# Performance work log

Hardware: AMD Instinct MI355X
Metric: run time of the kernel (lower is better)

The kernel has to match this reference:

```python
import jax, jax.numpy as jnp
import numpy as np

N = 65536      # total nodes (cells) in batch
E = 262144     # edges per edge type
T = 3          # edge types: row, col, diag
D = 128        # hidden_dim
HG = 4         # gat_heads
DHG = D // HG  # 32, GAT head dim
HH = 4         # hgt_heads
DHH = D // HH  # 32, HGT head dim
B = 32         # boards per batch
SLOPE = 0.2
EPS = 1e-6


def setup_inputs():
    ks = jax.random.split(jax.random.key(0), 32)
    def nrm(i, shape, s=0.05):
        return (jax.random.normal(ks[i], shape) * s).astype(jnp.float32)
    inp = {
        'x_cell': nrm(0, (N, D), 1.0),
        'z_h': nrm(1, (B, D), 1.0),
        'x_cell_embedded': nrm(2, (N, D), 1.0),
        'edge_index': jax.random.randint(ks[3], (T, 2, E), 0, N, dtype=jnp.int32),
        'batch_size': B,
        # GAT conv 1 (one GATConv per edge type, summed)
        'gat1_W': nrm(4, (T, D, D), 0.09),
        'gat1_asrc': nrm(5, (T, HG, DHG), 0.12),
        'gat1_adst': nrm(6, (T, HG, DHG), 0.12),
        'gat1_b': jnp.zeros((T, D), jnp.float32),
        # GAT conv 2
        'gat2_W': nrm(7, (T, D, D), 0.09),
        'gat2_asrc': nrm(8, (T, HG, DHG), 0.12),
        'gat2_adst': nrm(9, (T, HG, DHG), 0.12),
        'gat2_b': jnp.zeros((T, D), jnp.float32),
        # RMSNorms
        'norm1_s': jnp.ones((D,), jnp.float32),
        'norm2_s': jnp.ones((D,), jnp.float32),
        'norm3_s': jnp.ones((D,), jnp.float32),
        # HGT (single node type 'cell', T edge types)
        'hgt_Wk': nrm(10, (D, D), 0.09), 'hgt_bk': jnp.zeros((D,), jnp.float32),
        'hgt_Wq': nrm(11, (D, D), 0.09), 'hgt_bq': jnp.zeros((D,), jnp.float32),
        'hgt_Wv': nrm(12, (D, D), 0.09), 'hgt_bv': jnp.zeros((D,), jnp.float32),
        'hgt_arel': nrm(13, (T, HH, DHH, DHH), 0.15),
        'hgt_mrel': nrm(14, (T, HH, DHH, DHH), 0.15),
        'hgt_prel': jnp.ones((T, HH), jnp.float32),
        'hgt_Wo': nrm(15, (D, D), 0.09), 'hgt_bo': jnp.zeros((D,), jnp.float32),
        'hgt_skip': jnp.ones((), jnp.float32),
        # input injection
        'inj_W': nrm(16, (D, D), 0.09), 'inj_b': jnp.zeros((D,), jnp.float32),
        # FiLM
        'film_W1': nrm(17, (D, 2 * D), 0.09), 'film_b1': jnp.zeros((2 * D,), jnp.float32),
        'film_W2': nrm(18, (2 * D, 2 * D), 0.001), 'film_b2': jnp.zeros((2 * D,), jnp.float32),
    }
    return inp


def _rmsnorm(x, scale):
    return scale * x * jax.lax.rsqrt(jnp.mean(x * x, axis=-1, keepdims=True) + EPS)


def _res(x_old, x_new, scale):
    return jax.nn.leaky_relu(x_old + _rmsnorm(x_new, scale), SLOPE)


def _gat_sum(x, W, asrc, adst, b, src, dst):
    """HeteroConv(sum) over T GATConvs (concat heads, add_self_loops)."""
    loop = jnp.arange(N, dtype=src.dtype)
    def one(Wt, a_s, a_d, bt, s, t):
        s = jnp.concatenate([s, loop])   # self loops
        t = jnp.concatenate([t, loop])
        h = (x @ Wt).reshape(N, HG, DHG)             # [N,H,Dh]
        alpha_src = (h * a_s).sum(-1)                # [N,H]
        alpha_dst = (h * a_d).sum(-1)
        e = jax.nn.leaky_relu(alpha_src[s] + alpha_dst[t], SLOPE)  # [E+N,H]
        m = jax.ops.segment_max(e, t, num_segments=N)
        ex = jnp.exp(e - m[t])
        denom = jax.ops.segment_sum(ex, t, num_segments=N)
        alpha = ex / (denom[t] + 1e-16)
        out = jax.ops.segment_sum(alpha[:, :, None] * h[s], t, num_segments=N)
        return out.reshape(N, D) + bt
    return jax.vmap(one)(W, asrc, adst, b, src, dst).sum(0)


def _hgt(x, Wk, bk, Wq, bq, Wv, bv, a_rel, m_rel, p_rel, Wo, bo, skip, src, dst):
    k = (x @ Wk + bk).reshape(N, HH, DHH)
    q = (x @ Wq + bq).reshape(N, HH, DHH)
    v = (x @ Wv + bv).reshape(N, HH, DHH)
    # per-edge-type relation transforms at node level, then gather per edge
    k_t = jnp.einsum('nhd,thdf->tnhf', k, a_rel)    # [T,N,H,Dk]
    v_t = jnp.einsum('nhd,thdf->tnhf', v, m_rel)
    k_e = jax.vmap(lambda a, i: a[i])(k_t, src)     # [T,E,H,Dk]
    v_e = jax.vmap(lambda a, i: a[i])(v_t, src)
    score = (q[dst] * k_e).sum(-1) * p_rel[:, None, :] / np.sqrt(DHH)  # [T,E,H]
    score = score.reshape(T * E, HH)
    dst_f = dst.reshape(-1)
    m = jax.ops.segment_max(score, dst_f, num_segments=N)
    ex = jnp.exp(score - m[dst_f])
    denom = jax.ops.segment_sum(ex, dst_f, num_segments=N)
    alpha = ex / (denom[dst_f] + 1e-16)
    agg = jax.ops.segment_sum(alpha[:, :, None] * v_e.reshape(T * E, HH, DHH),
                              dst_f, num_segments=N)          # [N,H,Dk]
    out = jax.nn.gelu(agg.reshape(N, D), approximate=False) @ Wo + bo
    sig = jax.nn.sigmoid(skip)
    return sig * out + (1.0 - sig) * x


def _film(nodes, z_h, W1, b1, W2, b2, bsz):
    gb = jax.nn.gelu(z_h @ W1 + b1, approximate=False) @ W2 + b2  # [B,2D]
    gamma, beta = jnp.split(gb, 2, axis=-1)
    gamma = 0.1 * jnp.tanh(gamma)
    beta = 0.1 * jnp.tanh(beta)
    c = N // bsz
    out = (1.0 + gamma)[:, None, :] * nodes.reshape(bsz, c, D) + beta[:, None, :]
    return out.reshape(N, D)


def reference(x_cell, z_h, x_cell_embedded,
              gat1_W, gat1_asrc, gat1_adst, gat1_b,
              gat2_W, gat2_asrc, gat2_adst, gat2_b,
              norm1_s, norm2_s, norm3_s,
              hgt_Wk, hgt_bk, hgt_Wq, hgt_bq, hgt_Wv, hgt_bv,
              hgt_arel, hgt_mrel, hgt_prel, hgt_Wo, hgt_bo, hgt_skip,
              inj_W, inj_b, film_W1, film_b1, film_W2, film_b2,
              edge_index, batch_size):
    src = edge_index[:, 0]
    dst = edge_index[:, 1]
    x1 = _res(x_cell, _gat_sum(x_cell, gat1_W, gat1_asrc, gat1_adst, gat1_b, src, dst), norm1_s)
    x2 = _res(x1, _gat_sum(x1, gat2_W, gat2_asrc, gat2_adst, gat2_b, src, dst), norm2_s)
    x3 = _res(x2, _hgt(x2, hgt_Wk, hgt_bk, hgt_Wq, hgt_bq, hgt_Wv, hgt_bv,
                       hgt_arel, hgt_mrel, hgt_prel, hgt_Wo, hgt_bo, hgt_skip,
                       src, dst), norm3_s)
    x3 = x3 + x_cell_embedded @ inj_W + inj_b
    return _film(x3, z_h, film_W1, film_b1, film_W2, film_b2, batch_size)
```

## Files before the change

kernel.cpp:

```cpp
#include <hip/hip_runtime.h>

#define NN 65536
#define EE 262144
#define ND ((size_t)NN * 128)
#define TBW 132
#define WLP 136
#define NTOT (EE + NN)
#define CSRN (3*EE + 3*NN)

typedef unsigned short u16;
typedef short bf8_t __attribute__((ext_vector_type(8)));
typedef float f32x4 __attribute__((ext_vector_type(4)));

__device__ __forceinline__ float lrelu(float x){ return x > 0.f ? x : 0.2f*x; }
__device__ __forceinline__ float gelu_exact(float x){ return 0.5f*x*(1.f+erff(x*0.70710678118654752f)); }
__device__ __forceinline__ float fexp(float x){ return __expf(x); }
__device__ __forceinline__ u16 f2bf(float f){
    union { float f; unsigned u; } v; v.f = f;
    unsigned u = v.u;
    return (u16)((u + 0x7FFFu + ((u >> 16) & 1u)) >> 16);
}
__device__ __forceinline__ float bf2f(u16 b){
    union { unsigned u; float f; } v; v.u = ((unsigned)b) << 16; return v.f;
}
__device__ __forceinline__ float2 bf2x(unsigned p){
    union { unsigned u; float f; } a, b;
    a.u = (p & 0xFFFFu) << 16; b.u = p & 0xFFFF0000u;
    return make_float2(a.f, b.f);
}
__device__ __forceinline__ unsigned cvt2(float a, float b){
    unsigned r; asm("v_cvt_pk_bf16_f32 %0, %1, %2" : "=v"(r) : "v"(a), "v"(b)); return r;
}

__device__ __forceinline__ void load_af32(const float* __restrict__ X, int row, int lk, bf8_t* af){
    #pragma unroll
    for (int kk = 0; kk < 4; ++kk){
        const float* p = X + (size_t)row*128 + kk*32 + lk*8;
        float4 a = *(const float4*)p;
        float4 b = *(const float4*)(p+4);
        union { bf8_t v; unsigned u[4]; } r;
        r.u[0] = cvt2(a.x, a.y); r.u[1] = cvt2(a.z, a.w);
        r.u[2] = cvt2(b.x, b.y); r.u[3] = cvt2(b.z, b.w);
        af[kk] = r.v;
    }
}
__device__ __forceinline__ void load_af16(const u16* __restrict__ X, int row, int lk, bf8_t* af){
    #pragma unroll
    for (int kk = 0; kk < 4; ++kk)
        af[kk] = *(const bf8_t*)(X + (size_t)row*128 + kk*32 + lk*8);
}

__device__ __forceinline__ void stage_w(const u16* __restrict__ src, u16* __restrict__ wl, int tid){
    #pragma unroll
    for (int j = 0; j < 8; ++j){
        int o = (j*256 + tid)*8;
        bf8_t v = *(const bf8_t*)(src + o);
        *(bf8_t*)(wl + ((o>>7)*WLP + (o&127))) = v;
    }
}

__device__ __forceinline__ void mfma_l1_acc(const bf8_t* af, const u16* __restrict__ wl,
                                            int lr, int lk, f32x4* acc){
    #pragma unroll
    for (int kk = 0; kk < 4; ++kk){
        bf8_t B[8];
        #pragma unroll
        for (int nt = 0; nt < 8; ++nt)
            B[nt] = *(const bf8_t*)&wl[(nt*16+lr)*WLP + kk*32 + lk*8];
        #pragma unroll
        for (int nt = 0; nt < 8; ++nt)
            acc[nt] = __builtin_amdgcn_mfma_f32_16x16x32_bf16(af[kk], B[nt], acc[nt], 0, 0, 0);
    }
}
__device__ __forceinline__ void mfma_l1(const bf8_t* af, const u16* __restrict__ wl,
                                        int lr, int lk, f32x4* acc){
    #pragma unroll
    for (int i = 0; i < 8; ++i) acc[i] = (f32x4){0.f,0.f,0.f,0.f};
    mfma_l1_acc(af, wl, lr, lk, acc);
}
__device__ __forceinline__ void mfma_l2(const bf8_t* af0, const bf8_t* af1,
                                        const u16* __restrict__ wl,
                                        int lr, int lk, f32x4* acc0, f32x4* acc1){
    #pragma unroll
    for (int i = 0; i < 8; ++i){ acc0[i] = (f32x4){0.f,0.f,0.f,0.f}; acc1[i] = (f32x4){0.f,0.f,0.f,0.f}; }
    #pragma unroll
    for (int kk = 0; kk < 4; ++kk){
        bf8_t B[8];
        #pragma unroll
        for (int nt = 0; nt < 8; ++nt)
            B[nt] = *(const bf8_t*)&wl[(nt*16+lr)*WLP + kk*32 + lk*8];
        #pragma unroll
        for (int nt = 0; nt < 8; ++nt){
            acc0[nt] = __builtin_amdgcn_mfma_f32_16x16x32_bf16(af0[kk], B[nt], acc0[nt], 0, 0, 0);
            acc1[nt] = __builtin_amdgcn_mfma_f32_16x16x32_bf16(af1[kk], B[nt], acc1[nt], 0, 0, 0);
        }
    }
}

__device__ __forceinline__ void acc_to_tb(u16 (*tbw)[TBW], const f32x4* acc, int lr, int lk, const float* bias){
    asm volatile("s_waitcnt lgkmcnt(0)" ::: "memory");
    #pragma unroll
    for (int nt = 0; nt < 8; ++nt){
        int col = nt*16 + lr;
        float badd = bias ? bias[col] : 0.f;
        #pragma unroll
        for (int i = 0; i < 4; ++i) tbw[lk*4+i][col] = f2bf(acc[nt][i] + badd);
    }
    asm volatile("s_waitcnt lgkmcnt(0)" ::: "memory");
}
__device__ __forceinline__ void acc_to_tb_gelu(u16 (*tbw)[TBW], const f32x4* acc, int lr, int lk){
    asm volatile("s_waitcnt lgkmcnt(0)" ::: "memory");
    #pragma unroll
    for (int nt = 0; nt < 8; ++nt){
        int col = nt*16 + lr;
        #pragma unroll
        for (int i = 0; i < 4; ++i) tbw[lk*4+i][col] = f2bf(gelu_exact(acc[nt][i]));
    }
    asm volatile("s_waitcnt lgkmcnt(0)" ::: "memory");
}
__device__ __forceinline__ void tb_store(const u16 (*tbw)[TBW], u16* __restrict__ O, size_t rowstride, int rowbase, int lr, int lk){
    #pragma unroll
    for (int c = 0; c < 4; ++c){
        bf8_t v = *(const bf8_t*)&tbw[c*4+lk][lr*8];
        *(bf8_t*)(O + (size_t)(rowbase + c*4 + lk)*rowstride + lr*8) = v;
    }
}
__device__ __forceinline__ void tb_frags(const u16 (*tbw)[TBW], int lr, int lk, bf8_t* ha){
    #pragma unroll
    for (int kk = 0; kk < 4; ++kk) ha[kk] = *(const bf8_t*)&tbw[lr][kk*32 + lk*8];
}
__device__ __forceinline__ void tb_rows(const u16 (*tbw)[TBW], int lr, int lk, bf8_t* rw){
    #pragma unroll
    for (int c = 0; c < 4; ++c) rw[c] = *(const bf8_t*)&tbw[c*4+lk][lr*8];
}

__global__ __launch_bounds__(256) void wpack_k(
    const float* __restrict__ g1W, const float* __restrict__ g2W,
    const float* __restrict__ Wk, const float* __restrict__ Wq, const float* __restrict__ Wv,
    const float* __restrict__ Wo, const float* __restrict__ injW,
    const float* __restrict__ arel, const float* __restrict__ mrel,
    const float* __restrict__ g1as, const float* __restrict__ g1ad,
    const float* __restrict__ g2as, const float* __restrict__ g2ad,
    u16* __restrict__ wp, u16* __restrict__ wpa)
{
    int b = blockIdx.x, tid = threadIdx.x;
    if (b < 17) {
        const float* src; int rel = 0;
        if (b < 3) src = g1W + b*16384;
        else if (b < 6) src = g2W + (b-3)*16384;
        else if (b == 6) src = Wk;
        else if (b == 7) src = Wq;
        else if (b == 8) src = Wv;
        else if (b == 9) src = Wo;
        else if (b == 10) src = injW;
        else if (b < 14) { src = arel + (b-11)*4096; rel = 2; }
        else { src = mrel + (b-14)*4096; rel = 1; }
        u16* dst = wp + (size_t)b*16384;
        for (int idx = tid; idx < 16384; idx += 256) {
            int n = idx >> 7, k = idx & 127;
            float v;
            if (rel == 1)      v = ((n>>5)==(k>>5)) ? src[(n>>5)*1024 + (k&31)*32 + (n&31)] : 0.f;
            else if (rel == 2) v = ((n>>5)==(k>>5)) ? src[(n>>5)*1024 + (n&31)*32 + (k&31)] : 0.f;
            else               v = src[k*128 + n];
            dst[idx] = f2bf(v);
        }
    } else {
        for (int idx = tid; idx < 6*2048; idx += 256) {
            int m = idx >> 11;
            int j = idx & 2047;
            int cg = j >> 7, k = j & 127;
            const float* as = (m < 3) ? g1as : g2as;
            const float* ad = (m < 3) ? g1ad : g2ad;
            int t = (m < 3) ? m : m - 3;
            float v = 0.f;
            if (cg < 4)      { if ((k>>5)==cg)   v = as[t*128 + cg*32 + (k&31)]; }
            else if (cg < 8) { int g = cg-4; if ((k>>5)==g) v = ad[t*128 + g*32 + (k&31)]; }
            wpa[idx] = f2bf(v);
        }
    }
}

template<int AF32>
__global__ __launch_bounds__(256, 3) void gat_gemm3_k(const float* __restrict__ Xf, const u16* __restrict__ Xb,
    const u16* __restrict__ wpg, const u16* __restrict__ wpa,
    u16* __restrict__ hb, float* __restrict__ alsb, float* __restrict__ aldb)
{
    __shared__ __align__(16) u16 wl[128*WLP];
    __shared__ __align__(16) u16 tb[4][16][TBW];
    const int tid = threadIdx.x, wave = tid>>6, lane = tid&63, lr = lane&15, lk = lane>>4;
    const int t = blockIdx.y;
    const int rw0 = blockIdx.x*128 + wave*32;
    bf8_t af0[4], af1[4];
    if (AF32){ load_af32(Xf, rw0 + lr, lk, af0); load_af32(Xf, rw0 + 16 + lr, lk, af1); }
    else     { load_af16(Xb, rw0 + lr, lk, af0); load_af16(Xb, rw0 + 16 + lr, lk, af1); }
    stage_w(wpg + t*16384, wl, tid);
    bf8_t Ba[4];
    #pragma unroll
    for (int kk = 0; kk < 4; ++kk)
        Ba[kk] = *(const bf8_t*)&wpa[t*2048 + lr*128 + kk*32 + lk*8];
    __syncthreads();
    f32x4 acc0[8], acc1[8];
    mfma_l2(af0, af1, wl, lr, lk, acc0, acc1);
    u16* h = hb + (size_t)t*ND;
    float* alst = alsb + (size_t)t*NN*4;
    float* aldt = aldb + (size_t)t*NN*4;
    {
        acc_to_tb(tb[wave], acc0, lr, lk, nullptr);
        tb_store(tb[wave], h, 128, rw0, lr, lk);
        bf8_t ha[4]; tb_frags(tb[wave], lr, lk, ha);
        f32x4 a2 = (f32x4){0.f,0.f,0.f,0.f};
        #pragma unroll
        for (int kk = 0; kk < 4; ++kk)
            a2 = __builtin_amdgcn_mfma_f32_16x16x32_bf16(ha[kk], Ba[kk], a2, 0, 0, 0);
        if (lr < 8){
            float* dp = (lr < 4) ? alst : aldt;
            int g = lr & 3;
            #pragma unroll
            for (int i = 0; i < 4; ++i) dp[(size_t)(rw0 + lk*4 + i)*4 + g] = a2[i];
        }
    }
    {
        acc_to_tb(tb[wave], acc1, lr, lk, nullptr);
        tb_store(tb[wave], h, 128, rw0 + 16, lr, lk);
        bf8_t ha[4]; tb_frags(tb[wave], lr, lk, ha);
        f32x4 a2 = (f32x4){0.f,0.f,0.f,0.f};
        #pragma unroll
        for (int kk = 0; kk < 4; ++kk)
            a2 = __builtin_amdgcn_mfma_f32_16x16x32_bf16(ha[kk], Ba[kk], a2, 0, 0, 0);
        if (lr < 8){
            float* dp = (lr < 4) ? alst : aldt;
            int g = lr & 3;
            #pragma unroll
            for (int i = 0; i < 4; ++i) dp[(size_t)(rw0 + 16 + lk*4 + i)*4 + g] = a2[i];
        }
    }
}

__global__ __launch_bounds__(256, 3) void hgt_proj_k(const u16* __restrict__ X,
    const u16* __restrict__ wpk, const u16* __restrict__ wpq, const u16* __restrict__ wpv,
    const u16* __restrict__ wparel,
    const float* __restrict__ bk, const float* __restrict__ bq, const float* __restrict__ bv,
    u16* __restrict__ kvb, u16* __restrict__ qtb)
{
    __shared__ __align__(16) u16 wl[128*WLP];
    __shared__ __align__(16) u16 tb[4][16][TBW];
    const int tid = threadIdx.x, wave = tid>>6, lane = tid&63, lr = lane&15, lk = lane>>4;
    const int task = blockIdx.y;
    const int rw0 = blockIdx.x*128 + wave*32;
    bf8_t af0[4], af1[4];
    load_af16(X, rw0 + lr, lk, af0);
    load_af16(X, rw0 + 16 + lr, lk, af1);
    f32x4 acc0[8], acc1[8];
    if (task == 0) {
        stage_w(wpk, wl, tid);
        __syncthreads();
        mfma_l2(af0, af1, wl, lr, lk, acc0, acc1);
        acc_to_tb(tb[wave], acc0, lr, lk, bk); tb_store(tb[wave], kvb, 256, rw0, lr, lk);
        acc_to_tb(tb[wave], acc1, lr, lk, bk); tb_store(tb[wave], kvb, 256, rw0 + 16, lr, lk);
    } else if (task == 1) {
        stage_w(wpv, wl, tid);
        __syncthreads();
        mfma_l2(af0, af1, wl, lr, lk, acc0, acc1);
        acc_to_tb(tb[wave], acc0, lr, lk, bv); tb_store(tb[wave], kvb + 128, 256, rw0, lr, lk);
        acc_to_tb(tb[wave], acc1, lr, lk, bv); tb_store(tb[wave], kvb + 128, 256, rw0 + 16, lr, lk);
    } else {
        const int t = task - 2;
        stage_w(wpq, wl, tid);
        __syncthreads();
        mfma_l2(af0, af1, wl, lr, lk, acc0, acc1);
        bf8_t ha0[4], ha1[4];
        acc_to_tb(tb[wave], acc0, lr, lk, bq); tb_frags(tb[wave], lr, lk, ha0);
        acc_to_tb(tb[wave], acc1, lr, lk, bq); tb_frags(tb[wave], lr, lk, ha1);
        __syncthreads();
        stage_w(wparel + t*16384, wl, tid);
        __syncthreads();
        mfma_l2(ha0, ha1, wl, lr, lk, acc0, acc1);
        u16* o = qtb + (size_t)t*ND;
        acc_to_tb(tb[wave], acc0, lr, lk, nullptr); tb_store(tb[wave], o, 128, rw0, lr, lk);
        acc_to_tb(tb[wave], acc1, lr, lk, nullptr); tb_store(tb[wave], o, 128, rw0 + 16, lr, lk);
    }
}

__global__ __launch_bounds__(256) void hist_k(const int* __restrict__ ei, int* __restrict__ cnt){
    int gid = blockIdx.x*256 + threadIdx.x;
    int t = gid / EE, e = gid - t*EE;
    int d = ei[t*2*EE + EE + e];
    atomicAdd(&cnt[t*NN + d], 1);
}
__global__ __launch_bounds__(256) void scanA_k(const int* __restrict__ cnt, int* __restrict__ s0off, int* __restrict__ parts){
    __shared__ int sums[256];
    int b = blockIdx.x; int base = b * 1024;
    int tid = threadIdx.x;
    int v[4]; int tsum = 0;
    #pragma unroll
    for (int i = 0; i < 4; ++i){
        int n = base + tid*4 + i;
        v[i] = cnt[n] + cnt[NN+n] + cnt[2*NN+n] + 3;
        tsum += v[i];
    }
    sums[tid] = tsum; __syncthreads();
    for (int ofs = 1; ofs < 256; ofs <<= 1) {
        int a = (tid >= ofs) ? sums[tid-ofs] : 0;
        __syncthreads();
        sums[tid] += a;
        __syncthreads();
    }
    int run = sums[tid] - tsum;
    #pragma unroll
    for (int i = 0; i < 4; ++i){ s0off[base + tid*4 + i] = run; run += v[i]; }
    if (tid == 255) parts[b] = sums[255];
}
__global__ void scan2_k(int* parts){
    if (threadIdx.x == 0 && blockIdx.x == 0) {
        int run = 0;
        for (int i = 0; i < 64; ++i) { int v = parts[i]; parts[i] = run; run += v; }
    }
}
__global__ __launch_bounds__(256) void scanB_k(const int* __restrict__ cnt, int* __restrict__ s0off,
                                               int* __restrict__ s1off, int* __restrict__ s2off,
                                               const int* __restrict__ parts){
    int b = blockIdx.x; int base = b * 1024;
    int add = parts[b];
    #pragma unroll
    for (int i = 0; i < 4; ++i){
        int n = base + threadIdx.x*4 + i;
        int m = s0off[n] + add;
        int c0 = cnt[n], c1 = cnt[NN+n];
        s0off[n] = m;
        s1off[n] = m + c0 + 1;
        s2off[n] = m + c0 + c1 + 2;
    }
    if (b == 0 && threadIdx.x == 0) s0off[NN] = CSRN;
}
__global__ __launch_bounds__(256) void selffill_k(const int* __restrict__ s0off, const int* __restrict__ s1off,
                                                  const int* __restrict__ s2off, int* __restrict__ csrc){
    int gid = blockIdx.x*256 + threadIdx.x;
    int t = gid / NN, n = gid - t*NN;
    int pos = (t==0) ? s0off[n] : (t==1 ? s1off[n] : s2off[n]);
    csrc[pos] = n;
}
__global__ __launch_bounds__(256) void scatter_k(const int* __restrict__ ei,
    const int* __restrict__ s0off, const int* __restrict__ s1off, const int* __restrict__ s2off,
    int* __restrict__ cur, int* __restrict__ csrc, int* __restrict__ posmap){
    int gid = blockIdx.x*256 + threadIdx.x;
    int t = gid / EE, e = gid - t*EE;
    int s = ei[t*2*EE + e];
    int d = ei[t*2*EE + EE + e];
    int p = atomicAdd(&cur[t*NN + d], 1);
    int basep = (t==0) ? s0off[d] : (t==1 ? s1off[d] : s2off[d]);
    int pos = basep + 1 + p;
    csrc[pos] = s;
    posmap[t*EE + e] = pos;
}

__global__ __launch_bounds__(256) void alpha_k(const float* __restrict__ alsb, const float* __restrict__ aldb,
    const int* __restrict__ ei, const int* __restrict__ posmap,
    const int* __restrict__ s0off, const int* __restrict__ s1off, const int* __restrict__ s2off,
    float4* __restrict__ ab)
{
    int gid = blockIdx.x*256 + threadIdx.x;
    int t = gid / NTOT, r = gid - t*NTOT;
    int s, d, pos;
    if (r < EE) {
        s = ei[t*2*EE + r];
        d = ei[t*2*EE + EE + r];
        pos = posmap[t*EE + r];
    } else {
        int n = r - EE;
        s = n; d = n;
        pos = (t==0) ? s0off[n] : (t==1 ? s1off[n] : s2off[n]);
    }
    const float* As = alsb + ((size_t)t*NN + s)*4;
    const float* Ad = aldb + ((size_t)t*NN + d)*4;
    float4 o;
    o.x = fexp(lrelu(As[0] + Ad[0]));
    o.y = fexp(lrelu(As[1] + Ad[1]));
    o.z = fexp(lrelu(As[2] + Ad[2]));
    o.w = fexp(lrelu(As[3] + Ad[3]));
    ab[pos] = o;
}

template<int XF32>
__global__ __launch_bounds__(256) void gat_aggres_k(const u16* __restrict__ hb,
    const float* __restrict__ abf,
    const int* __restrict__ s0off, const int* __restrict__ s1off, const int* __restrict__ s2off,
    const int* __restrict__ csrc,
    const float* __restrict__ bias3, const float* __restrict__ xoldf, const u16* __restrict__ xoldb,
    const float* __restrict__ scale, u16* __restrict__ outb)
{
    int gid = blockIdx.x*256 + threadIdx.x;
    int node = gid >> 6, lane = gid & 63;
    int g = lane >> 4;
    int segb[4] = { s0off[node], s1off[node], s2off[node], s0off[node+1] };
    float a0 = 0.f, a1 = 0.f;
    for (int t = 0; t < 3; ++t) {
        const u16* h = hb + (size_t)t*ND;
        int beg = segb[t], end = segb[t+1];
        float s0 = 0.f, s1 = 0.f, ds = 0.f;
        for (int pos = beg; pos < end; pos += 4) {
            int pc[4]; float al[4]; int sp[4]; unsigned hw[4];
            #pragma unroll
            for (int j = 0; j < 4; ++j){
                int pj = pos + j;
                pc[j] = (pj < end) ? pj : beg;
            }
            #pragma unroll
            for (int j = 0; j < 4; ++j) sp[j] = csrc[pc[j]];
            #pragma unroll
            for (int j = 0; j < 4; ++j){
                float a = abf[(size_t)pc[j]*4 + g];
                al[j] = (pos + j < end) ? a : 0.f;
                hw[j] = *(const unsigned*)&h[(size_t)sp[j]*128 + lane*2];
            }
            #pragma unroll
            for (int j = 0; j < 4; ++j){
                float2 w = bf2x(hw[j]);
                ds += al[j]; s0 += al[j]*w.x; s1 += al[j]*w.y;
            }
        }
        float inv = 1.f/(ds + 1e-16f);
        a0 += s0*inv; a1 += s1*inv;
    }
    int c0 = lane*2;
    a0 += bias3[c0]   + bias3[128+c0]   + bias3[256+c0];
    a1 += bias3[c0+1] + bias3[128+c0+1] + bias3[256+c0+1];
    float ssum = a0*a0 + a1*a1;
    #pragma unroll
    for (int o = 1; o < 64; o <<= 1) ssum += __shfl_xor(ssum, o);
    float r = rsqrtf(ssum*(1.f/128.f) + 1e-6f);
    size_t off = (size_t)node*128 + c0;
    float2 xo;
    if (XF32) xo = *(const float2*)&xoldf[off];
    else      xo = bf2x(*(const unsigned*)&xoldb[off]);
    float y0 = lrelu(xo.x + scale[c0]*a0*r);
    float y1 = lrelu(xo.y + scale[c0+1]*a1*r);
    *(unsigned*)&outb[off] = cvt2(y0, y1);
}

__global__ __launch_bounds__(256) void hgt_agg_k(const u16* __restrict__ kvb,
    const u16* __restrict__ qtb, const float* __restrict__ prel,
    const int* __restrict__ s0off, const int* __restrict__ s1off, const int* __restrict__ s2off,
    const int* __restrict__ csrc, u16* __restrict__ pb)
{
    int gid = blockIdx.x*256 + threadIdx.x;
    int node = gid >> 6, lane = gid & 63;
    int hh = lane >> 4;
    const float S = 0.17677669529663689f;
    int segb[4] = { s0off[node], s1off[node], s2off[node], s0off[node+1] };
    float dsum = 0.f;
    float a0[3], a1[3];
    for (int t = 0; t < 3; ++t) {
        a0[t] = 0.f; a1[t] = 0.f;
        float ph = prel[t*4 + hh] * S;
        float2 qv = bf2x(*(const unsigned*)&qtb[(size_t)t*ND + (size_t)node*128 + lane*2]);
        int beg = segb[t] + 1, end = segb[t+1];
        for (int pos = beg; pos < end; pos += 4) {
            int pc[4]; int sp[4]; unsigned kw[4], vw[4];
            #pragma unroll
            for (int j = 0; j < 4; ++j){
                int pj = pos + j;
                pc[j] = (pj < end) ? pj : beg;
            }
            #pragma unroll
            for (int j = 0; j < 4; ++j) sp[j] = csrc[pc[j]];
            #pragma unroll
            for (int j = 0; j < 4; ++j){
                size_t ro = (size_t)sp[j]*256 + lane*2;
                kw[j] = *(const unsigned*)&kvb[ro];
                vw[j] = *(const unsigned*)&kvb[ro + 128];
            }
            float sc[4];
            #pragma unroll
            for (int j = 0; j < 4; ++j){
                float2 k2 = bf2x(kw[j]);
                sc[j] = qv.x*k2.x + qv.y*k2.y;
            }
            #pragma unroll
            for (int o = 1; o < 16; o <<= 1){
                #pragma unroll
                for (int j = 0; j < 4; ++j) sc[j] += __shfl_xor(sc[j], o);
            }
            #pragma unroll
            for (int j = 0; j < 4; ++j){
                float ex = (pos + j < end) ? fexp(sc[j]*ph) : 0.f;
                float2 v2 = bf2x(vw[j]);
                dsum += ex; a0[t] += ex*v2.x; a1[t] += ex*v2.y;
            }
        }
    }
    float inv = 1.f/(dsum + 1e-16f);
    size_t o = (size_t)node*128 + lane*2;
    *(unsigned*)&pb[o]        = cvt2(a0[0]*inv, a1[0]*inv);
    *(unsigned*)&pb[ND + o]   = cvt2(a0[1]*inv, a1[1]*inv);
    *(unsigned*)&pb[2*ND + o] = cvt2(a0[2]*inv, a1[2]*inv);
}

__global__ __launch_bounds__(256, 3) void final_k(const u16* __restrict__ pb,
    const u16* __restrict__ wpmrel, const u16* __restrict__ wpo, const float* __restrict__ bo,
    const u16* __restrict__ x2b, const float* __restrict__ skipp, const float* __restrict__ scale,
    const float* __restrict__ xemb, const u16* __restrict__ wpinj, const float* __restrict__ injb,
    const float* __restrict__ gbuf, const int* __restrict__ bszp,
    float* __restrict__ out)
{
    __shared__ __align__(16) u16 wl[128*WLP];
    __shared__ __align__(16) u16 tb[4][16][TBW];
    const int tid = threadIdx.x, wave = tid>>6, lane = tid&63, lr = lane&15, lk = lane>>4;
    const int rw = blockIdx.x*64 + wave*16;
    f32x4 acc[8];
    #pragma unroll
    for (int i = 0; i < 8; ++i) acc[i] = (f32x4){0.f,0.f,0.f,0.f};
    for (int t = 0; t < 3; ++t){
        if (t) __syncthreads();
        bf8_t a0[4]; load_af16(pb + (size_t)t*ND, rw + lr, lk, a0);
        stage_w(wpmrel + t*16384, wl, tid);
        __syncthreads();
        mfma_l1_acc(a0, wl, lr, lk, acc);
    }
    bf8_t ga[4];
    acc_to_tb_gelu(tb[wave], acc, lr, lk);
    tb_frags(tb[wave], lr, lk, ga);
    __syncthreads();
    stage_w(wpo, wl, tid);
    __syncthreads();
    mfma_l1(ga, wl, lr, lk, acc);
    bf8_t hw[4];
    acc_to_tb(tb[wave], acc, lr, lk, bo);
    tb_rows(tb[wave], lr, lk, hw);
    bf8_t e0[4];
    load_af32(xemb, rw + lr, lk, e0);
    __syncthreads();
    stage_w(wpinj, wl, tid);
    __syncthreads();
    mfma_l1(e0, wl, lr, lk, acc);
    bf8_t in[4];
    acc_to_tb(tb[wave], acc, lr, lk, injb);
    tb_rows(tb[wave], lr, lk, in);
    const float sig = 1.f/(1.f + expf(-skipp[0]));
    const int cpb = NN / *bszp;
    float4 sca = *(const float4*)&scale[lr*8];
    float4 scb = *(const float4*)&scale[lr*8 + 4];
    #pragma unroll
    for (int c = 0; c < 4; ++c){
        int row = rw + c*4 + lk;
        bf8_t x8 = *(const bf8_t*)(x2b + (size_t)row*128 + lr*8);
        float x[8], v[8];
        float ssl = 0.f;
        #pragma unroll
        for (int j = 0; j < 8; ++j){
            x[j] = bf2f((u16)x8[j]);
            float h = bf2f((u16)hw[c][j]);
            v[j] = sig*h + (1.f - sig)*x[j];
            ssl += v[j]*v[j];
        }
        ssl += __shfl_xor(ssl, 1); ssl += __shfl_xor(ssl, 2);
        ssl += __shfl_xor(ssl, 4); ssl += __shfl_xor(ssl, 8);
        float rq = rsqrtf(ssl*(1.f/128.f) + 1e-6f);
        const float* gr = gbuf + (row / cpb)*256;
        float4 g0 = *(const float4*)&gr[lr*8];
        float4 g1 = *(const float4*)&gr[lr*8 + 4];
        float4 b0 = *(const float4*)&gr[128 + lr*8];
        float4 b1 = *(const float4*)&gr[128 + lr*8 + 4];
        float4 oA, oB;
        #pragma unroll
        for (int j = 0; j < 8; ++j){
            float scj = (j < 4) ? ((const float*)&sca)[j] : ((const float*)&scb)[j-4];
            float y = lrelu(x[j] + scj*v[j]*rq);
            float hf = y + bf2f((u16)in[c][j]);
            float gj = (j < 4) ? ((const float*)&g0)[j] : ((const float*)&g1)[j-4];
            float bj = (j < 4) ? ((const float*)&b0)[j] : ((const float*)&b1)[j-4];
            float ov = (1.f + gj)*hf + bj;
            if (j < 4) ((float*)&oA)[j] = ov; else ((float*)&oB)[j-4] = ov;
        }
        *(float4*)(out + (size_t)row*128 + lr*8)     = oA;
        *(float4*)(out + (size_t)row*128 + lr*8 + 4) = oB;
    }
}

__global__ __launch_bounds__(256) void film_k(const float* __restrict__ z,
    const float* __restrict__ W1, const float* __restrict__ b1,
    const float* __restrict__ W2, const float* __restrict__ b2,
    float* __restrict__ gb)
{
    __shared__ float zr[128];
    __shared__ float g1[256];
    int r = blockIdx.x, tid = threadIdx.x;
    if (tid < 128) zr[tid] = z[r*128 + tid];
    __syncthreads();
    float s = b1[tid];
    for (int k = 0; k < 128; ++k) s += zr[k]*W1[k*256 + tid];
    g1[tid] = gelu_exact(s);
    __syncthreads();
    float s2 = b2[tid];
    for (int k = 0; k < 256; ++k) s2 += g1[k]*W2[k*256 + tid];
    gb[r*256 + tid] = 0.1f*tanhf(s2);
}

extern "C" void kernel_launch(void* const* d_in, const int* in_sizes, int n_in,
                              void* d_out, int out_size, void* d_ws, size_t ws_size,
                              hipStream_t stream)
{
    const float* x_cell = (const float*)d_in[0];
    const float* z_h    = (const float*)d_in[1];
    const float* x_emb  = (const float*)d_in[2];
    const int*   eidx   = (const int*)d_in[3];
    const int*   bszp   = (const int*)d_in[4];
    const float* g1W  = (const float*)d_in[5];
    const float* g1as = (const float*)d_in[6];
    const float* g1ad = (const float*)d_in[7];
    const float* g1b  = (const float*)d_in[8];
    const float* g2W  = (const float*)d_in[9];
    const float* g2as = (const float*)d_in[10];
    const float* g2ad = (const float*)d_in[11];
    const float* g2b  = (const float*)d_in[12];
    const float* n1s  = (const float*)d_in[13];
    const float* n2s  = (const float*)d_in[14];
    const float* n3s  = (const float*)d_in[15];
    const float* Wk   = (const float*)d_in[16];
    const float* bk   = (const float*)d_in[17];
    const float* Wq   = (const float*)d_in[18];
    const float* bq   = (const float*)d_in[19];
    const float* Wv   = (const float*)d_in[20];
    const float* bv   = (const float*)d_in[21];
    const float* arel = (const float*)d_in[22];
    const float* mrel = (const float*)d_in[23];
    const float* prel = (const float*)d_in[24];
    const float* Wo   = (const float*)d_in[25];
    const float* bo   = (const float*)d_in[26];
    const float* skipp= (const float*)d_in[27];
    const float* injW = (const float*)d_in[28];
    const float* injb = (const float*)d_in[29];
    const float* fW1  = (const float*)d_in[30];
    const float* fb1  = (const float*)d_in[31];
    const float* fW2  = (const float*)d_in[32];
    const float* fb2  = (const float*)d_in[33];

    u16* wp   = (u16*)d_ws;
    u16* wpa  = wp + (size_t)17*16384;
    float4* ab = (float4*)(wpa + 6*2048);
    u16* x1b  = (u16*)(ab + CSRN);
    u16* x2b  = x1b + ND;
    u16* kvb  = x2b + ND;
    u16* pb   = kvb + 2*ND;
    u16* hb   = pb + 3*ND;
    float* alsb = (float*)(hb + 3*ND);
    float* aldb = alsb + (size_t)3*NN*4;
    float* gbuf = aldb + (size_t)3*NN*4;
    int* s0off  = (int*)(gbuf + 32*256);
    int* s1off  = s0off + (NN+1);
    int* s2off  = s1off + NN;
    int* csrc   = s2off + NN;
    int* posmap = csrc + CSRN;
    int* tmpc   = posmap + 3*EE;
    int* cur    = tmpc + 3*NN;
    int* parts  = cur + 3*NN;

    u16* qtb = hb;
    float* outp = (float*)d_out;

    const u16* wpg1 = wp;
    const u16* wpg2 = wp + (size_t)3*16384;
    const u16* wpk  = wp + (size_t)6*16384;
    const u16* wpq  = wp + (size_t)7*16384;
    const u16* wpv  = wp + (size_t)8*16384;
    const u16* wpo  = wp + (size_t)9*16384;
    const u16* wpinj= wp + (size_t)10*16384;
    const u16* wparel = wp + (size_t)11*16384;
    const u16* wpmrel = wp + (size_t)14*16384;

    wpack_k<<<18, 256, 0, stream>>>(g1W, g2W, Wk, Wq, Wv, Wo, injW, arel, mrel,
                                    g1as, g1ad, g2as, g2ad, wp, wpa);

    hipMemsetAsync(tmpc, 0, 3*NN*sizeof(int), stream);
    hist_k<<<3*EE/256, 256, 0, stream>>>(eidx, tmpc);
    scanA_k<<<64, 256, 0, stream>>>(tmpc, s0off, parts);
    scan2_k<<<1, 64, 0, stream>>>(parts);
    scanB_k<<<64, 256, 0, stream>>>(tmpc, s0off, s1off, s2off, parts);
    selffill_k<<<3*NN/256, 256, 0, stream>>>(s0off, s1off, s2off, csrc);
    hipMemsetAsync(cur, 0, 3*NN*sizeof(int), stream);
    scatter_k<<<3*EE/256, 256, 0, stream>>>(eidx, s0off, s1off, s2off, cur, csrc, posmap);

    int B = in_sizes[1] / 128;
    film_k<<<B, 256, 0, stream>>>(z_h, fW1, fb1, fW2, fb2, gbuf);

    gat_gemm3_k<1><<<dim3(512,3), 256, 0, stream>>>(x_cell, nullptr, wpg1, wpa, hb, alsb, aldb);
    alpha_k<<<3*NTOT/256, 256, 0, stream>>>(alsb, aldb, eidx, posmap, s0off, s1off, s2off, ab);
    gat_aggres_k<1><<<16384, 256, 0, stream>>>(hb, (const float*)ab, s0off, s1off, s2off, csrc,
                                               g1b, x_cell, nullptr, n1s, x1b);

    gat_gemm3_k<0><<<dim3(512,3), 256, 0, stream>>>(nullptr, x1b, wpg2, wpa + 3*2048, hb, alsb, aldb);
    alpha_k<<<3*NTOT/256, 256, 0, stream>>>(alsb, aldb, eidx, posmap, s0off, s1off, s2off, ab);
    gat_aggres_k<0><<<16384, 256, 0, stream>>>(hb, (const float*)ab, s0off, s1off, s2off, csrc,
                                               g2b, nullptr, x1b, n2s, x2b);

    hgt_proj_k<<<dim3(512,5), 256, 0, stream>>>(x2b, wpk, wpq, wpv, wparel,
                                                bk, bq, bv, kvb, qtb);
    hgt_agg_k<<<16384, 256, 0, stream>>>(kvb, qtb, prel, s0off, s1off, s2off, csrc, pb);

    final_k<<<1024, 256, 0, stream>>>(pb, wpmrel, wpo, bo, x2b, skipp, n3s,
                                      x_emb, wpinj, injb, gbuf, bszp, outp);
}
```

Measured before the change: 583.7 us.

## Split each wavefront across two edges per step with 4 channels per lane

The GAT and HGT aggregation kernels now have each 64-lane wavefront process two edges at once. Each half-wave handles 32 lanes, and each lane covers 4 channels loaded as 8-byte vectors instead of 2 channels as 4-byte loads. The two half-wave partial sums are combined with a cross-half shuffle at the end. This widens the per-lane gathers, shortens the HGT score reduction from 4 shuffle steps to 3, and issues more independent edge loads per iteration. In exchange it adds extra shuffles and more registers per lane, and padding can waste work when edge counts are odd.

```diff
diff --git a/kernel.cpp b/kernel.cpp
--- a/kernel.cpp
+++ b/kernel.cpp
@@ -390,51 +390,71 @@
 {
     int gid = blockIdx.x*256 + threadIdx.x;
     int node = gid >> 6, lane = gid & 63;
-    int g = lane >> 4;
+    int eh = lane >> 5, hh = (lane >> 3) & 3, cp = lane & 7;
+    int ch = hh*32 + cp*4;
     int segb[4] = { s0off[node], s1off[node], s2off[node], s0off[node+1] };
-    float a0 = 0.f, a1 = 0.f;
+    float a[4] = {0.f, 0.f, 0.f, 0.f};
+    #pragma unroll
     for (int t = 0; t < 3; ++t) {
         const u16* h = hb + (size_t)t*ND;
         int beg = segb[t], end = segb[t+1];
-        float s0 = 0.f, s1 = 0.f, ds = 0.f;
+        float ds = 0.f, s0 = 0.f, s1 = 0.f, s2 = 0.f, s3 = 0.f;
         for (int pos = beg; pos < end; pos += 4) {
-            int pc[4]; float al[4]; int sp[4]; unsigned hw[4];
-            #pragma unroll
-            for (int j = 0; j < 4; ++j){
-                int pj = pos + j;
-                pc[j] = (pj < end) ? pj : beg;
-            }
-            #pragma unroll
-            for (int j = 0; j < 4; ++j) sp[j] = csrc[pc[j]];
-            #pragma unroll
-            for (int j = 0; j < 4; ++j){
-                float a = abf[(size_t)pc[j]*4 + g];
-                al[j] = (pos + j < end) ? a : 0.f;
-                hw[j] = *(const unsigned*)&h[(size_t)sp[j]*128 + lane*2];
-            }
-            #pragma unroll
-            for (int j = 0; j < 4; ++j){
-                float2 w = bf2x(hw[j]);
-                ds += al[j]; s0 += al[j]*w.x; s1 += al[j]*w.y;
-            }
-        }
+            int p0 = pos + eh, p1 = pos + 2 + eh;
+            int v0 = (p0 < end), v1 = (p1 < end);
+            int q0 = v0 ? p0 : beg, q1 = v1 ? p1 : beg;
+            int sA = csrc[q0], sB = csrc[q1];
+            float alA = abf[(size_t)q0*4 + hh];
+            float alB = abf[(size_t)q1*4 + hh];
+            uint2 hA = *(const uint2*)&h[(size_t)sA*128 + ch];
+            uint2 hB = *(const uint2*)&h[(size_t)sB*128 + ch];
+            alA = v0 ? alA : 0.f;
+            alB = v1 ? alB : 0.f;
+            float2 wA0 = bf2x(hA.x), wA1 = bf2x(hA.y);
+            float2 wB0 = bf2x(hB.x), wB1 = bf2x(hB.y);
+            ds += alA + alB;
+            s0 += alA*wA0.x + alB*wB0.x;
+            s1 += alA*wA0.y + alB*wB0.y;
+            s2 += alA*wA1.x + alB*wB1.x;
+            s3 += alA*wA1.y + alB*wB1.y;
+        }
+        ds += __shfl_xor(ds, 32);
+        s0 += __shfl_xor(s0, 32);
+        s1 += __shfl_xor(s1, 32);
+        s2 += __shfl_xor(s2, 32);
+        s3 += __shfl_xor(s3, 32);
         float inv = 1.f/(ds + 1e-16f);
-        a0 += s0*inv; a1 += s1*inv;
-    }
-    int c0 = lane*2;
-    a0 += bias3[c0]   + bias3[128+c0]   + bias3[256+c0];
-    a1 += bias3[c0+1] + bias3[128+c0+1] + bias3[256+c0+1];
-    float ssum = a0*a0 + a1*a1;
-    #pragma unroll
-    for (int o = 1; o < 64; o <<= 1) ssum += __shfl_xor(ssum, o);
+        a[0] += s0*inv; a[1] += s1*inv; a[2] += s2*inv; a[3] += s3*inv;
+    }
+    float4 b0 = *(const float4*)&bias3[ch];
+    float4 b1 = *(const float4*)&bias3[128 + ch];
+    float4 b2 = *(const float4*)&bias3[256 + ch];
+    a[0] += b0.x + b1.x + b2.x;
+    a[1] += b0.y + b1.y + b2.y;
+    a[2] += b0.z + b1.z + b2.z;
+    a[3] += b0.w + b1.w + b2.w;
+    float ssum = a[0]*a[0] + a[1]*a[1] + a[2]*a[2] + a[3]*a[3];
+    ssum += __shfl_xor(ssum, 1); ssum += __shfl_xor(ssum, 2);
+    ssum += __shfl_xor(ssum, 4); ssum += __shfl_xor(ssum, 8);
+    ssum += __shfl_xor(ssum, 16);
     float r = rsqrtf(ssum*(1.f/128.f) + 1e-6f);
-    size_t off = (size_t)node*128 + c0;
-    float2 xo;
-    if (XF32) xo = *(const float2*)&xoldf[off];
-    else      xo = bf2x(*(const unsigned*)&xoldb[off]);
-    float y0 = lrelu(xo.x + scale[c0]*a0*r);
-    float y1 = lrelu(xo.y + scale[c0+1]*a1*r);
-    *(unsigned*)&outb[off] = cvt2(y0, y1);
+    float4 sc = *(const float4*)&scale[ch];
+    size_t off = (size_t)node*128 + ch;
+    float x0, x1v, x2v, x3;
+    if (XF32) {
+        float4 xo = *(const float4*)&xoldf[off];
+        x0 = xo.x; x1v = xo.y; x2v = xo.z; x3 = xo.w;
+    } else {
+        uint2 xo = *(const uint2*)&xoldb[off];
+        float2 p0 = bf2x(xo.x), p1 = bf2x(xo.y);
+        x0 = p0.x; x1v = p0.y; x2v = p1.x; x3 = p1.y;
+    }
+    float y0 = lrelu(x0  + sc.x*a[0]*r);
+    float y1 = lrelu(x1v + sc.y*a[1]*r);
+    float y2 = lrelu(x2v + sc.z*a[2]*r);
+    float y3 = lrelu(x3  + sc.w*a[3]*r);
+    uint2 o2; o2.x = cvt2(y0, y1); o2.y = cvt2(y2, y3);
+    *(uint2*)&outb[off] = o2;
 }
 
 __global__ __launch_bounds__(256) void hgt_agg_k(const u16* __restrict__ kvb,
@@ -444,55 +464,64 @@
 {
     int gid = blockIdx.x*256 + threadIdx.x;
     int node = gid >> 6, lane = gid & 63;
-    int hh = lane >> 4;
+    int eh = lane >> 5, hh = (lane >> 3) & 3, cp = lane & 7;
+    int ch = hh*32 + cp*4;
     const float S = 0.17677669529663689f;
     int segb[4] = { s0off[node], s1off[node], s2off[node], s0off[node+1] };
     float dsum = 0.f;
-    float a0[3], a1[3];
+    float ac[3][4];
+    #pragma unroll
+    for (int t = 0; t < 3; ++t){ ac[t][0]=0.f; ac[t][1]=0.f; ac[t][2]=0.f; ac[t][3]=0.f; }
+    #pragma unroll
     for (int t = 0; t < 3; ++t) {
-        a0[t] = 0.f; a1[t] = 0.f;
         float ph = prel[t*4 + hh] * S;
-        float2 qv = bf2x(*(const unsigned*)&qtb[(size_t)t*ND + (size_t)node*128 + lane*2]);
-        int beg = segb[t] + 1, end = segb[t+1];
+        uint2 qw = *(const uint2*)&qtb[(size_t)t*ND + (size_t)node*128 + ch];
+        float2 q0 = bf2x(qw.x), q1 = bf2x(qw.y);
+        int self = segb[t];
+        int beg = self + 1, end = segb[t+1];
         for (int pos = beg; pos < end; pos += 4) {
-            int pc[4]; int sp[4]; unsigned kw[4], vw[4];
-            #pragma unroll
-            for (int j = 0; j < 4; ++j){
-                int pj = pos + j;
-                pc[j] = (pj < end) ? pj : beg;
-            }
-            #pragma unroll
-            for (int j = 0; j < 4; ++j) sp[j] = csrc[pc[j]];
-            #pragma unroll
-            for (int j = 0; j < 4; ++j){
-                size_t ro = (size_t)sp[j]*256 + lane*2;
-                kw[j] = *(const unsigned*)&kvb[ro];
-                vw[j] = *(const unsigned*)&kvb[ro + 128];
-            }
-            float sc[4];
-            #pragma unroll
-            for (int j = 0; j < 4; ++j){
-                float2 k2 = bf2x(kw[j]);
-                sc[j] = qv.x*k2.x + qv.y*k2.y;
-            }
-            #pragma unroll
-            for (int o = 1; o < 16; o <<= 1){
-                #pragma unroll
-                for (int j = 0; j < 4; ++j) sc[j] += __shfl_xor(sc[j], o);
-            }
-            #pragma unroll
-            for (int j = 0; j < 4; ++j){
-                float ex = (pos + j < end) ? fexp(sc[j]*ph) : 0.f;
-                float2 v2 = bf2x(vw[j]);
-                dsum += ex; a0[t] += ex*v2.x; a1[t] += ex*v2.y;
-            }
-        }
+            int p0 = pos + eh, p1 = pos + 2 + eh;
+            int v0 = (p0 < end), v1 = (p1 < end);
+            int qp0 = v0 ? p0 : self, qp1 = v1 ? p1 : self;
+            int sA = csrc[qp0], sB = csrc[qp1];
+            size_t rA = (size_t)sA*256 + ch, rB = (size_t)sB*256 + ch;
+            uint2 kA = *(const uint2*)&kvb[rA], kB = *(const uint2*)&kvb[rB];
+            uint2 vA = *(const uint2*)&kvb[rA + 128], vB = *(const uint2*)&kvb[rB + 128];
+            float2 kA0 = bf2x(kA.x), kA1 = bf2x(kA.y);
+            float2 kB0 = bf2x(kB.x), kB1 = bf2x(kB.y);
+            float scA = kA0.x*q0.x + kA0.y*q0.y + kA1.x*q1.x + kA1.y*q1.y;
+            float scB = kB0.x*q0.x + kB0.y*q0.y + kB1.x*q1.x + kB1.y*q1.y;
+            scA += __shfl_xor(scA, 1); scB += __shfl_xor(scB, 1);
+            scA += __shfl_xor(scA, 2); scB += __shfl_xor(scB, 2);
+            scA += __shfl_xor(scA, 4); scB += __shfl_xor(scB, 4);
+            float eA = v0 ? fexp(scA*ph) : 0.f;
+            float eB = v1 ? fexp(scB*ph) : 0.f;
+            float2 vA0 = bf2x(vA.x), vA1 = bf2x(vA.y);
+            float2 vB0 = bf2x(vB.x), vB1 = bf2x(vB.y);
+            dsum += eA + eB;
+            ac[t][0] += eA*vA0.x + eB*vB0.x;
+            ac[t][1] += eA*vA0.y + eB*vB0.y;
+            ac[t][2] += eA*vA1.x + eB*vB1.x;
+            ac[t][3] += eA*vA1.y + eB*vB1.y;
+        }
+    }
+    dsum += __shfl_xor(dsum, 32);
+    #pragma unroll
+    for (int t = 0; t < 3; ++t){
+        ac[t][0] += __shfl_xor(ac[t][0], 32);
+        ac[t][1] += __shfl_xor(ac[t][1], 32);
+        ac[t][2] += __shfl_xor(ac[t][2], 32);
+        ac[t][3] += __shfl_xor(ac[t][3], 32);
     }
     float inv = 1.f/(dsum + 1e-16f);
-    size_t o = (size_t)node*128 + lane*2;
-    *(unsigned*)&pb[o]        = cvt2(a0[0]*inv, a1[0]*inv);
-    *(unsigned*)&pb[ND + o]   = cvt2(a0[1]*inv, a1[1]*inv);
-    *(unsigned*)&pb[2*ND + o] = cvt2(a0[2]*inv, a1[2]*inv);
+    size_t o = (size_t)node*128 + ch;
+    #pragma unroll
+    for (int t = 0; t < 3; ++t){
+        uint2 o2;
+        o2.x = cvt2(ac[t][0]*inv, ac[t][1]*inv);
+        o2.y = cvt2(ac[t][2]*inv, ac[t][3]*inv);
+        *(uint2*)&pb[(size_t)t*ND + o] = o2;
+    }
 }
 
 __global__ __launch_bounds__(256, 3) void final_k(const u16* __restrict__ pb,
```

Result: no change. 588.9 us (+0.9%).
